# Optimization experiments

Measured on AMD Instinct MI355X. Metric: run time of the kernel, lower is better.

Reference implementation:

```python
import jax, jax.numpy as jnp
import numpy as np

H = 128  # target_size / hidden_size
D_IN = 2  # input_size - 2 (stard_LSTM slices off last 2 grid coords)
SAMP = 10  # sampling_num (hardcoded stride 10 in forward loop)


def lstm_encode(x, lengths, W_ih, W_hh, b_ih, b_hh):
    # x: [B, T, D_IN]; torch.nn.LSTMCell math, zero initial state
    B, T, _ = x.shape
    xg = jnp.einsum('btd,gd->btg', x, W_ih) + b_ih  # precompute input projections [B,T,4H]

    def step(carry, xt):
        h, c = carry
        g = xt + h @ W_hh.T + b_hh
        i, f, gg, o = jnp.split(g, 4, axis=-1)
        c = jax.nn.sigmoid(f) * c + jax.nn.sigmoid(i) * jnp.tanh(gg)
        h = jax.nn.sigmoid(o) * jnp.tanh(c)
        return (h, c), h

    h0 = jnp.zeros((B, H), x.dtype)
    _, hs = jax.lax.scan(step, (h0, h0), xg.transpose(1, 0, 2))
    outputs = hs.transpose(1, 0, 2)  # [B, T, H]
    emb = outputs[jnp.arange(B), jnp.clip(lengths - 1, 0)]  # last valid step per sequence
    return emb, outputs


def gather_sub(tensor, sub_len):
    # tensor: [B, T, H]; sub_len: [B*SAMP]; row k reads tensor[k//SAMP, sub_len[k]-1]
    rows = jnp.arange(sub_len.shape[0]) // SAMP
    return tensor[rows, jnp.clip(sub_len - 1, 0)]


def exp_neg_dist(a, b):
    return jnp.exp(-jnp.sqrt(jnp.sum((a - b) ** 2, axis=-1)))


def setup_inputs() -> dict:
    key = jax.random.key(0)
    ks = jax.random.split(key, 12)
    B, T, D = 220, 512, 4
    NS = B * SAMP
    rint = lambda k, n: jnp.maximum(jax.random.randint(k, (n,), 0, T), 1).astype(jnp.int64)
    inp = {
        'traj_input': jax.random.normal(ks[0], (B, T, D), jnp.float32),
        'traj_length': rint(ks[1], B),
        'traj_anchor_sub_length': rint(ks[2], NS),
        'traj_farest_sub_length': rint(ks[3], NS),
        'traj_anchor_input': jax.random.normal(ks[4], (B, T, D), jnp.float32),
        'traj_anchor_length': rint(ks[5], B),
        'anchor_sub_length': rint(ks[6], NS),
        'traj_farest_input': jax.random.normal(ks[7], (B, T, D), jnp.float32),
        'traj_farest_length': rint(ks[8], B),
        'farest_sub_length': rint(ks[9], NS),
        'W_ih': jax.random.normal(ks[10], (4 * H, D_IN), jnp.float32) / np.sqrt(H),
        'W_hh': jax.random.normal(ks[11], (4 * H, H), jnp.float32) / np.sqrt(H),
        'b_ih': jnp.zeros((4 * H,), jnp.float32),
        'b_hh': jnp.zeros((4 * H,), jnp.float32),
    }
    return inp


def reference(traj_input, traj_length, traj_anchor_sub_length, traj_farest_sub_length,
              traj_anchor_input, traj_anchor_length, anchor_sub_length,
              traj_farest_input, traj_farest_length, farest_sub_length,
              W_ih, W_hh, b_ih, b_hh):
    # stard_LSTM=True path: cell input drops last 2 coords
    t_emb, t_out = lstm_encode(traj_input[..., :-2], traj_length, W_ih, W_hh, b_ih, b_hh)
    a_emb, a_out = lstm_encode(traj_anchor_input[..., :-2], traj_anchor_length, W_ih, W_hh, b_ih, b_hh)
    f_emb, f_out = lstm_encode(traj_farest_input[..., :-2], traj_farest_length, W_ih, W_hh, b_ih, b_hh)

    ta_sub = gather_sub(t_out, traj_anchor_sub_length)
    tf_sub = gather_sub(t_out, traj_farest_sub_length)
    an_sub = gather_sub(a_out, anchor_sub_length)
    fa_sub = gather_sub(f_out, farest_sub_length)

    anchor_distance = exp_neg_dist(t_emb, a_emb)
    farest_distance = exp_neg_dist(t_emb, f_emb)
    anchor_sub_distance = exp_neg_dist(ta_sub, an_sub)
    farest_sub_distance = exp_neg_dist(tf_sub, fa_sub)
    return (anchor_distance, farest_distance, anchor_sub_distance, farest_sub_distance)
```

## Files before the change

### kernel.cpp

```cpp
#include <hip/hip_runtime.h>

#define H    128
#define T    512
#define DX   4
#define BB   220
#define SAMP 10
#define NS   (BB*SAMP)
#define M    4
#define NBLK 55
#define MAXSLOT 84

typedef _Float16 half8 __attribute__((ext_vector_type(8)));
typedef float    f32x4 __attribute__((ext_vector_type(4)));

#define WS_TEMB 0
#define WS_AEMB (WS_TEMB + BB*H)
#define WS_FEMB (WS_AEMB + BB*H)
#define WS_TA   (WS_FEMB + BB*H)
#define WS_TF   (WS_TA + NS*H)
#define WS_AN   (WS_TF + NS*H)
#define WS_FA   (WS_AN + NS*H)
#define WS_FLAGS (WS_FA + NS*H)

#define LOG2E  1.442695041f
#define LOG2E2 2.885390082f

__device__ static inline float bf2f(unsigned short u) {
  unsigned int i = ((unsigned int)u) << 16;
  return __builtin_bit_cast(float, i);
}
__device__ static inline unsigned short f2bf(float f) {
  unsigned int i = __builtin_bit_cast(unsigned int, f);
  i += 0x7fffu + ((i >> 16) & 1u);
  return (unsigned short)(i >> 16);
}
__device__ static inline float loadF(const void* p, size_t i, int isbf) {
  return isbf ? bf2f(((const unsigned short*)p)[i]) : ((const float*)p)[i];
}
__device__ static inline int loadI(const void* p, int i, int is64) {
  return is64 ? (int)((const unsigned int*)p)[2*(size_t)i] : ((const int*)p)[i];
}
__device__ static inline float frcp(float x) { return __builtin_amdgcn_rcpf(x); }
__device__ static inline float ex2(float x)  { return __builtin_amdgcn_exp2f(x); }
__device__ static inline float sigmY(float y)  { return frcp(1.f + ex2(-y)); }
__device__ static inline float tanhY(float y)  { return 1.f - 2.f*frcp(1.f + ex2(y)); }
__device__ static inline float scrub(float x) { return (x == x) ? x : 0.f; }
__device__ static inline int clampT(int v) { v = v - 1; if (v < 0) v = 0; if (v > T-1) v = T-1; return v; }

__global__ __launch_bounds__(512, 2) void lstm_scan(
    const void* __restrict__ x0_, const void* __restrict__ len0,
    const void* __restrict__ sub_ta, const void* __restrict__ sub_tf,
    const void* __restrict__ x1_, const void* __restrict__ len1,
    const void* __restrict__ sub_an,
    const void* __restrict__ x2_, const void* __restrict__ len2,
    const void* __restrict__ sub_fa,
    const void* __restrict__ Wih, const void* __restrict__ Whh,
    const void* __restrict__ bih, const void* __restrict__ bhh,
    float* __restrict__ ws)
{
  const int e      = blockIdx.y;
  const int s0     = blockIdx.x * M;
  const int tid    = threadIdx.x;
  const int lane   = tid & 63;
  const int w      = tid >> 6;
  const int lo     = lane & 15;
  const int quad   = lane >> 4;

  int fbf, f64;
  {
    const unsigned int* wp = (const unsigned int*)Whh;
    int cnt = 0;
    for (int i = 0; i < 64; ++i) {
      unsigned int lo16 = wp[i] & 0xFFFFu;
      int ex = (int)((lo16 >> 7) & 0xFFu);
      cnt += (ex >= 100 && ex <= 130);
    }
    fbf = (cnt >= 40);
    const unsigned int* l = (const unsigned int*)len0;
    f64 = ((l[1] | l[3] | l[5] | l[7]) == 0u);
    if (blockIdx.x == 0 && blockIdx.y == 0 && tid == 0) {
      int* fo = (int*)(ws + WS_FLAGS); fo[0] = fbf; fo[1] = f64;
    }
  }

  const void* xin  = (e==0) ? x0_ : (e==1 ? x1_ : x2_);
  const void* lenp = (e==0) ? len0 : (e==1 ? len1 : len2);

  __shared__ __align__(16) _Float16 afr[2][4][16][8];
  __shared__ __align__(16) float2 xbf[M][T+2];
  __shared__ __align__(16) _Float16 sbuf[MAXSLOT][H];
  __shared__ int slot_off[MAXSLOT];

  ((unsigned int*)afr)[tid] = 0u;
  for (int i = tid; i < M*T; i += 512) {
    int m = i >> 9, t = i & (T-1);
    size_t base = ((size_t)(s0+m)*T + t) * DX;
    xbf[m][t] = make_float2(loadF(xin, base + 0, fbf), loadF(xin, base + 1, fbf));
  }
  half8 Bf[4][4];
  const int col = w*16 + lo;
  #pragma unroll
  for (int q = 0; q < 4; ++q) {
    const float sc = (q == 2) ? LOG2E2 : LOG2E;
    const int g = q*128 + col;
    #pragma unroll
    for (int kt = 0; kt < 4; ++kt) {
      #pragma unroll
      for (int j = 0; j < 8; ++j) {
        const int k = kt*32 + quad*8 + j;
        Bf[q][kt][j] = (_Float16)(sc * loadF(Whh, (size_t)g*H + k, fbf));
      }
    }
  }
  float wx0[4], wx1[4], bb[4];
  #pragma unroll
  for (int q = 0; q < 4; ++q) {
    const float sc = (q == 2) ? LOG2E2 : LOG2E;
    const int g = q*128 + col;
    wx0[q] = sc * loadF(Wih, (size_t)g*2 + 0, fbf);
    wx1[q] = sc * loadF(Wih, (size_t)g*2 + 1, fbf);
    bb[q]  = sc * (loadF(bih, g, fbf) + loadF(bhh, g, fbf));
  }
  const int nslots = (e == 0) ? M*21 : M*11;
  int myt = -2, mym = 0;
  if (e == 0) {
    if (tid < M*21) {
      int m = tid / 21, j = tid - m*21, sg = s0 + m;
      mym = m;
      int off;
      if (j == 0)       { myt = clampT(loadI(lenp, sg, f64));            off = WS_TEMB + sg*H; }
      else if (j <= 10) { int k = sg*10 + (j-1);  myt = clampT(loadI(sub_ta, k, f64)); off = WS_TA + k*H; }
      else              { int k = sg*10 + (j-11); myt = clampT(loadI(sub_tf, k, f64)); off = WS_TF + k*H; }
      slot_off[tid] = off;
    }
  } else {
    if (tid < M*11) {
      int m = tid / 11, j = tid - m*11, sg = s0 + m;
      mym = m;
      int off;
      if (j == 0) { myt = clampT(loadI(lenp, sg, f64)); off = (e==1 ? WS_AEMB : WS_FEMB) + sg*H; }
      else {
        int k = sg*10 + (j-1);
        if (e == 1) { myt = clampT(loadI(sub_an, k, f64)); off = WS_AN + k*H; }
        else        { myt = clampT(loadI(sub_fa, k, f64)); off = WS_FA + k*H; }
      }
      slot_off[tid] = off;
    }
  }
  __syncthreads();

  float cs = 0.f;
  const int rdchunk = quad*4 + (lo >> 2);
  const _Float16* rdb[2] = { &afr[0][0][rdchunk][0], &afr[1][0][rdchunk][0] };
  const _Float16* sbb[2] = { &afr[0][0][0][0], &afr[1][0][0][0] };
  const int wrkt    = w >> 1;
  const int wrchunk = ((w & 1)*2 + (lo >> 3))*4 + quad;
  const int wrj     = lo & 7;
  _Float16* wrb[2] = { &afr[0][wrkt][wrchunk][wrj], &afr[1][wrkt][wrchunk][wrj] };
  const float2* xrow = &xbf[quad][0];
  const int c0 = 2*lane;
  const int snap_base = (c0 >> 5)*128 + ((c0 >> 3) & 3)*32 + (c0 & 7);

  auto snap = [&](int tq, int rp) {
    unsigned long long mask = __ballot(myt == tq);
    if (mask) {
      const _Float16* sb = sbb[rp];
      do {
        int src = __ffsll((unsigned long long)mask) - 1;
        mask &= mask - 1;
        int m    = __shfl(mym, src);
        int slot = w*64 + src;
        unsigned int pk = *(const unsigned int*)(sb + snap_base + m*8);
        *(unsigned int*)&sbuf[slot][c0] = pk;
      } while (mask);
    }
  };

  auto step = [&](int rp, int wp, int t) {
    float2 xv = xrow[t];
    const _Float16* rb = rdb[rp];
    half8 A[4];
    #pragma unroll
    for (int kt = 0; kt < 4; ++kt)
      A[kt] = *(const half8*)(rb + kt*128);

    float pre[4];
    #pragma unroll
    for (int q = 0; q < 4; ++q)
      pre[q] = bb[q] + wx0[q]*xv.x + wx1[q]*xv.y;
    f32x4 G[4];
    #pragma unroll
    for (int q = 0; q < 4; ++q)
      G[q] = (f32x4){pre[q], pre[q], pre[q], pre[q]};

    __builtin_amdgcn_s_setprio(1);
    #pragma unroll
    for (int kt = 0; kt < 4; ++kt)
      #pragma unroll
      for (int q = 0; q < 4; ++q)
        G[q] = __builtin_amdgcn_mfma_f32_16x16x32_f16(A[kt], Bf[q][kt], G[q], 0, 0, 0);
    __builtin_amdgcn_s_setprio(0);

    snap(t-1, rp);

    float sf = sigmY(G[1][0]);
    float si = sigmY(G[0][0]);
    float tg = tanhY(G[2][0]);
    float ig = (si * tg) * LOG2E2;
    cs = sf*cs + ig;
    float tc = tanhY(cs);
    float so = sigmY(G[3][0]);
    *wrb[wp] = (_Float16)(so * tc);
    __syncthreads();
  };

  #pragma unroll 1
  for (int t = 0; t < T; t += 2) {
    step(0, 1, t);
    step(1, 0, t+1);
  }

  snap(T-1, 0);

  __syncthreads();
  for (int i = tid; i < nslots*64; i += 512) {
    int slot = i >> 6, c2 = i & 63;
    unsigned int pk = *(const unsigned int*)&sbuf[slot][2*c2];
    float2 v;
    v.x = (float)__builtin_bit_cast(_Float16, (unsigned short)(pk & 0xFFFFu));
    v.y = (float)__builtin_bit_cast(_Float16, (unsigned short)(pk >> 16));
    *(float2*)(ws + slot_off[slot] + 2*c2) = v;
  }
}

__global__ void dists(const float* __restrict__ ws, void* __restrict__ outv) {
  const int fbf = ((const int*)(ws + WS_FLAGS))[0];
  const int gtid = blockIdx.x*256 + threadIdx.x;
  const int widx = gtid >> 6, lane = gtid & 63;
  const float *pa, *pb;
  if (widx < 220)       { pa = ws + WS_TEMB + (size_t)widx*H;        pb = ws + WS_AEMB + (size_t)widx*H; }
  else if (widx < 440)  { int b = widx-220;  pa = ws + WS_TEMB + (size_t)b*H; pb = ws + WS_FEMB + (size_t)b*H; }
  else if (widx < 2640) { int k = widx-440;  pa = ws + WS_TA + (size_t)k*H;   pb = ws + WS_AN + (size_t)k*H; }
  else                  { int k = widx-2640; pa = ws + WS_TF + (size_t)k*H;   pb = ws + WS_FA + (size_t)k*H; }
  float d0 = pa[lane]    - pb[lane];
  float d1 = pa[lane+64] - pb[lane+64];
  float s  = scrub(d0*d0 + d1*d1);
  #pragma unroll
  for (int off = 32; off > 0; off >>= 1) s += __shfl_down(s, off, 64);
  if (lane == 0) {
    float r = __expf(-sqrtf(s));
    if (fbf) ((unsigned short*)outv)[widx] = f2bf(r);
    else     ((float*)outv)[widx] = r;
  }
}

extern "C" void kernel_launch(void* const* d_in, const int* in_sizes, int n_in,
                              void* d_out, int out_size, void* d_ws, size_t ws_size,
                              hipStream_t stream) {
  float* ws = (float*)d_ws;
  hipLaunchKernelGGL(lstm_scan, dim3(NBLK, 3), dim3(512), 0, stream,
                     d_in[0], d_in[1], d_in[2], d_in[3],
                     d_in[4], d_in[5], d_in[6],
                     d_in[7], d_in[8], d_in[9],
                     d_in[10], d_in[11], d_in[12], d_in[13], ws);
  hipLaunchKernelGGL(dists, dim3(4840*64/256), dim3(256), 0, stream, ws, d_out);
}
```

Measured before the change: 399.2 us.

## Halve waves per LSTM block, each wave computing two 16-column gate chunks

```diff
diff --git a/kernel.cpp b/kernel.cpp
--- a/kernel.cpp
+++ b/kernel.cpp
@@ -47,7 +47,7 @@
 __device__ static inline float scrub(float x) { return (x == x) ? x : 0.f; }
 __device__ static inline int clampT(int v) { v = v - 1; if (v < 0) v = 0; if (v > T-1) v = T-1; return v; }
 
-__global__ __launch_bounds__(512, 2) void lstm_scan(
+__global__ __launch_bounds__(256, 1) void lstm_scan(
     const void* __restrict__ x0_, const void* __restrict__ len0,
     const void* __restrict__ sub_ta, const void* __restrict__ sub_tf,
     const void* __restrict__ x1_, const void* __restrict__ len1,
@@ -91,35 +91,42 @@
   __shared__ __align__(16) _Float16 sbuf[MAXSLOT][H];
   __shared__ int slot_off[MAXSLOT];
 
-  ((unsigned int*)afr)[tid] = 0u;
-  for (int i = tid; i < M*T; i += 512) {
+  for (int i = tid; i < 512; i += 256) ((unsigned int*)afr)[i] = 0u;
+  for (int i = tid; i < M*T; i += 256) {
     int m = i >> 9, t = i & (T-1);
     size_t base = ((size_t)(s0+m)*T + t) * DX;
     xbf[m][t] = make_float2(loadF(xin, base + 0, fbf), loadF(xin, base + 1, fbf));
   }
-  half8 Bf[4][4];
-  const int col = w*16 + lo;
+  half8 Bf[2][4][4];
   #pragma unroll
-  for (int q = 0; q < 4; ++q) {
-    const float sc = (q == 2) ? LOG2E2 : LOG2E;
-    const int g = q*128 + col;
-    #pragma unroll
-    for (int kt = 0; kt < 4; ++kt) {
-      #pragma unroll
-      for (int j = 0; j < 8; ++j) {
-        const int k = kt*32 + quad*8 + j;
-        Bf[q][kt][j] = (_Float16)(sc * loadF(Whh, (size_t)g*H + k, fbf));
+  for (int ch = 0; ch < 2; ++ch) {
+    const int col = w*32 + ch*16 + lo;
+    #pragma unroll
+    for (int q = 0; q < 4; ++q) {
+      const float sc = (q == 2) ? LOG2E2 : LOG2E;
+      const int g = q*128 + col;
+      #pragma unroll
+      for (int kt = 0; kt < 4; ++kt) {
+        #pragma unroll
+        for (int j = 0; j < 8; ++j) {
+          const int k = kt*32 + quad*8 + j;
+          Bf[ch][q][kt][j] = (_Float16)(sc * loadF(Whh, (size_t)g*H + k, fbf));
+        }
       }
     }
   }
-  float wx0[4], wx1[4], bb[4];
+  float wx0[2][4], wx1[2][4], bb[2][4];
   #pragma unroll
-  for (int q = 0; q < 4; ++q) {
-    const float sc = (q == 2) ? LOG2E2 : LOG2E;
-    const int g = q*128 + col;
-    wx0[q] = sc * loadF(Wih, (size_t)g*2 + 0, fbf);
-    wx1[q] = sc * loadF(Wih, (size_t)g*2 + 1, fbf);
-    bb[q]  = sc * (loadF(bih, g, fbf) + loadF(bhh, g, fbf));
+  for (int ch = 0; ch < 2; ++ch) {
+    const int col = w*32 + ch*16 + lo;
+    #pragma unroll
+    for (int q = 0; q < 4; ++q) {
+      const float sc = (q == 2) ? LOG2E2 : LOG2E;
+      const int g = q*128 + col;
+      wx0[ch][q] = sc * loadF(Wih, (size_t)g*2 + 0, fbf);
+      wx1[ch][q] = sc * loadF(Wih, (size_t)g*2 + 1, fbf);
+      bb[ch][q]  = sc * (loadF(bih, g, fbf) + loadF(bhh, g, fbf));
+    }
   }
   const int nslots = (e == 0) ? M*21 : M*11;
   int myt = -2, mym = 0;
@@ -149,14 +156,13 @@
   }
   __syncthreads();
 
-  float cs = 0.f;
+  float cs[2] = {0.f, 0.f};
   const int rdchunk = quad*4 + (lo >> 2);
   const _Float16* rdb[2] = { &afr[0][0][rdchunk][0], &afr[1][0][rdchunk][0] };
   const _Float16* sbb[2] = { &afr[0][0][0][0], &afr[1][0][0][0] };
-  const int wrkt    = w >> 1;
-  const int wrchunk = ((w & 1)*2 + (lo >> 3))*4 + quad;
-  const int wrj     = lo & 7;
-  _Float16* wrb[2] = { &afr[0][wrkt][wrchunk][wrj], &afr[1][wrkt][wrchunk][wrj] };
+  _Float16* wrb[2][2] = {
+    { &afr[0][w][((lo>>3)  )*4+quad][lo&7], &afr[0][w][(2+(lo>>3))*4+quad][lo&7] },
+    { &afr[1][w][((lo>>3)  )*4+quad][lo&7], &afr[1][w][(2+(lo>>3))*4+quad][lo&7] } };
   const float2* xrow = &xbf[quad][0];
   const int c0 = 2*lane;
   const int snap_base = (c0 >> 5)*128 + ((c0 >> 3) & 3)*32 + (c0 & 7);
@@ -176,41 +182,58 @@
     }
   };
 
+  f32x4 G[2][4];
+  float2 xn;
+  {
+    float2 v0 = xrow[0];
+    #pragma unroll
+    for (int ch = 0; ch < 2; ++ch)
+      #pragma unroll
+      for (int q = 0; q < 4; ++q)
+        G[ch][q] = (f32x4){ bb[ch][q] + wx0[ch][q]*v0.x + wx1[ch][q]*v0.y, 0.f, 0.f, 0.f };
+    xn = xrow[1];
+  }
+
   auto step = [&](int rp, int wp, int t) {
-    float2 xv = xrow[t];
     const _Float16* rb = rdb[rp];
     half8 A[4];
     #pragma unroll
     for (int kt = 0; kt < 4; ++kt)
       A[kt] = *(const half8*)(rb + kt*128);
 
-    float pre[4];
-    #pragma unroll
-    for (int q = 0; q < 4; ++q)
-      pre[q] = bb[q] + wx0[q]*xv.x + wx1[q]*xv.y;
-    f32x4 G[4];
-    #pragma unroll
-    for (int q = 0; q < 4; ++q)
-      G[q] = (f32x4){pre[q], pre[q], pre[q], pre[q]};
-
-    __builtin_amdgcn_s_setprio(1);
     #pragma unroll
     for (int kt = 0; kt < 4; ++kt)
       #pragma unroll
+      for (int ch = 0; ch < 2; ++ch)
+        #pragma unroll
+        for (int q = 0; q < 4; ++q)
+          G[ch][q] = __builtin_amdgcn_mfma_f32_16x16x32_f16(A[kt], Bf[ch][q][kt], G[ch][q], 0, 0, 0);
+
+    float pan[2][4];
+    #pragma unroll
+    for (int ch = 0; ch < 2; ++ch)
+      #pragma unroll
       for (int q = 0; q < 4; ++q)
-        G[q] = __builtin_amdgcn_mfma_f32_16x16x32_f16(A[kt], Bf[q][kt], G[q], 0, 0, 0);
-    __builtin_amdgcn_s_setprio(0);
-
+        pan[ch][q] = bb[ch][q] + wx0[ch][q]*xn.x + wx1[ch][q]*xn.y;
+    xn = xrow[t+2];
     snap(t-1, rp);
 
-    float sf = sigmY(G[1][0]);
-    float si = sigmY(G[0][0]);
-    float tg = tanhY(G[2][0]);
-    float ig = (si * tg) * LOG2E2;
-    cs = sf*cs + ig;
-    float tc = tanhY(cs);
-    float so = sigmY(G[3][0]);
-    *wrb[wp] = (_Float16)(so * tc);
+    #pragma unroll
+    for (int ch = 0; ch < 2; ++ch) {
+      float sf = sigmY(G[ch][1][0]);
+      float si = sigmY(G[ch][0][0]);
+      float tg = tanhY(G[ch][2][0]);
+      float ig = (si * tg) * LOG2E2;
+      cs[ch] = sf*cs[ch] + ig;
+      float tc = tanhY(cs[ch]);
+      float so = sigmY(G[ch][3][0]);
+      *wrb[wp][ch] = (_Float16)(so * tc);
+    }
+    #pragma unroll
+    for (int ch = 0; ch < 2; ++ch)
+      #pragma unroll
+      for (int q = 0; q < 4; ++q)
+        G[ch][q][0] = pan[ch][q];
     __syncthreads();
   };
 
@@ -223,7 +246,7 @@
   snap(T-1, 0);
 
   __syncthreads();
-  for (int i = tid; i < nslots*64; i += 512) {
+  for (int i = tid; i < nslots*64; i += 256) {
     int slot = i >> 6, c2 = i & 63;
     unsigned int pk = *(const unsigned int*)&sbuf[slot][2*c2];
     float2 v;
@@ -258,7 +281,7 @@
                               void* d_out, int out_size, void* d_ws, size_t ws_size,
                               hipStream_t stream) {
   float* ws = (float*)d_ws;
-  hipLaunchKernelGGL(lstm_scan, dim3(NBLK, 3), dim3(512), 0, stream,
+  hipLaunchKernelGGL(lstm_scan, dim3(NBLK, 3), dim3(256), 0, stream,
                      d_in[0], d_in[1], d_in[2], d_in[3],
                      d_in[4], d_in[5], d_in[6],
                      d_in[7], d_in[8], d_in[9],
```

Result: slower. 417.2 us (+4.5%).
